# Optimization experiments

Measured on AMD Instinct MI355X. Metric: run time of the kernel, lower is better.

The kernel has to match this reference:

```python
import jax, jax.numpy as jnp
import numpy as np

NUM_FREQ = 64
DIM_OUTPUT = 512
CONST_INV_SOFTMAX = 1e-05


def setup_inputs() -> dict:
    key = jax.random.key(0)
    k1, k2, k3 = jax.random.split(key, 3)
    dim_input = 1024
    L = NUM_FREQ + 1
    batch = jax.random.normal(k1, (16, 4096, dim_input), dtype=jnp.float32)
    # nn.Linear default init (~U[-1/sqrt(fan_in), 1/sqrt(fan_in)]) then divided by 100
    bound = 1.0 / np.sqrt(dim_input)
    W = jax.random.uniform(k2, (2 * L, dim_input), minval=-bound, maxval=bound, dtype=jnp.float32) / 100.0
    b = jax.random.uniform(k3, (2 * L,), minval=-bound, maxval=bound, dtype=jnp.float32) / 100.0
    return {"batch": batch, "W": W, "b": b}


def _autocorrelate(a):
    # a: [B, L] complex. r[k] = sum_j a[j+k] * conj(a[j]), k = 0..L-1.
    # Equivalent to the grouped conv1d in the original; computed via zero-padded FFT.
    L = a.shape[-1]
    X = jnp.fft.fft(a, n=2 * L, axis=-1)
    r = jnp.fft.ifft(X * jnp.conj(X), axis=-1)
    return r[:, :L]


def reference(batch, W, b):
    L = NUM_FREQ + 1
    shape_out = batch.shape[:-1] + (DIM_OUTPUT,)
    x = batch.reshape(-1, batch.shape[-1])              # [B, d_in]
    p = x @ W.T + b                                      # [B, 2L]
    a = jax.lax.complex(p[:, :L], p[:, L:])              # [B, L] complex64
    r = _autocorrelate(a)                                # [B, L] fourier coeffs
    c = r[:, 1:] / r[:, :1].real                         # normalized coeffs [B, F]
    # bin centerpoints on [-1, 1]
    edges = jnp.linspace(-1.0, 1.0, DIM_OUTPUT + 1)
    centers = (edges[:-1] + edges[1:]) / 2               # [D]
    freqs = jnp.pi * jnp.arange(1, L, dtype=jnp.float32) # [F]
    phase = centers[:, None] * freqs[None, :]            # [D, F]
    # Re( sum_f c[b,f] * exp(i*phase[d,f]) ) = c.re @ cos - c.im @ sin
    like = 0.5 + c.real @ jnp.cos(phase).T - c.imag @ jnp.sin(phase).T  # [B, D]
    dist = like / jnp.sum(like, axis=-1, keepdims=True)
    logits = jnp.log(dist + CONST_INV_SOFTMAX)
    return logits.reshape(shape_out)
```

## Files before the change

### kernel.cpp

```cpp
#include <hip/hip_runtime.h>
#include <hip/hip_bf16.h>
#include <math.h>

#define BDIM 1024
#define NP   130
#define LL   65
#define NPAD 144
#define KP2  160
#define DOUT 512

typedef __attribute__((ext_vector_type(4))) float f32x4;
typedef __attribute__((ext_vector_type(8))) __bf16 bf16x8;

__global__ void fill_wbf(const float* __restrict__ W, __bf16* __restrict__ Wbf) {
  int idx = blockIdx.x * 256 + threadIdx.x;
  int c = idx >> 10, k = idx & 1023;
  float v = (c < NP) ? W[c * BDIM + k] : 0.f;
  Wbf[idx] = (__bf16)v;
}

__global__ void fill_mt(__bf16* __restrict__ Mt) {
  int idx = blockIdx.x * 256 + threadIdx.x;
  int col = idx / KP2, k = idx - col * KP2;
  int d = col >> 1, im = col & 1;
  float v = 0.f;
  if (k < NP) {
    int j = (k < LL) ? k : k - LL;
    double theta = M_PI * (-1.0 + (2.0 * (double)d + 1.0) / 512.0);
    double ph = (double)j * theta;
    double s = sin(ph), c = cos(ph);
    v = (float)((k < LL) ? (im ? s : c) : (im ? c : -s));
  }
  Mt[idx] = (__bf16)v;
}

__global__ __launch_bounds__(256) void gemm1(
    const float* __restrict__ X, const __bf16* __restrict__ Wbf,
    const float* __restrict__ bias, __bf16* __restrict__ P,
    float* __restrict__ R0) {
  const int tid  = threadIdx.x;
  const int w    = tid >> 6;
  const int lane = tid & 63;
  const int l15  = lane & 15;
  const int quad = lane >> 4;
  const long rowbase = (long)blockIdx.x * 128 + w * 32;

  f32x4 acc[2][9];
#pragma unroll
  for (int rt = 0; rt < 2; rt++)
#pragma unroll
    for (int j = 0; j < 9; j++) acc[rt][j] = (f32x4){0.f, 0.f, 0.f, 0.f};

  const float*  xptr = X   + (rowbase + l15) * BDIM + quad * 8;
  const __bf16* wptr = Wbf + (long)l15 * BDIM + quad * 8;

  for (int k0 = 0; k0 < BDIM; k0 += 32) {
    bf16x8 a[2];
#pragma unroll
    for (int rt = 0; rt < 2; rt++) {
      f32x4 x0 = *(const f32x4*)(xptr + (long)rt * 16 * BDIM + k0);
      f32x4 x1 = *(const f32x4*)(xptr + (long)rt * 16 * BDIM + k0 + 4);
      bf16x8 af;
      af[0] = (__bf16)x0[0]; af[1] = (__bf16)x0[1];
      af[2] = (__bf16)x0[2]; af[3] = (__bf16)x0[3];
      af[4] = (__bf16)x1[0]; af[5] = (__bf16)x1[1];
      af[6] = (__bf16)x1[2]; af[7] = (__bf16)x1[3];
      a[rt] = af;
    }
#pragma unroll
    for (int j = 0; j < 9; j++) {
      bf16x8 b = *(const bf16x8*)(wptr + (long)j * 16 * BDIM + k0);
      acc[0][j] = __builtin_amdgcn_mfma_f32_16x16x32_bf16(a[0], b, acc[0][j], 0, 0, 0);
      acc[1][j] = __builtin_amdgcn_mfma_f32_16x16x32_bf16(a[1], b, acc[1][j], 0, 0, 0);
    }
  }

  float s[2][4];
#pragma unroll
  for (int rt = 0; rt < 2; rt++)
#pragma unroll
    for (int reg = 0; reg < 4; reg++) s[rt][reg] = 0.f;

#pragma unroll
  for (int j = 0; j < 9; j++) {
    int c = j * 16 + l15;
    float bj = (c < NP) ? bias[c] : 0.f;
#pragma unroll
    for (int rt = 0; rt < 2; rt++) {
#pragma unroll
      for (int reg = 0; reg < 4; reg++) {
        long row = rowbase + rt * 16 + quad * 4 + reg;
        float pv = acc[rt][j][reg] + bj;
        if (c >= NP) pv = 0.f;
        P[row * KP2 + c] = (__bf16)pv;
        s[rt][reg] = fmaf(pv, pv, s[rt][reg]);
      }
    }
  }
#pragma unroll
  for (int rt = 0; rt < 2; rt++)
#pragma unroll
    for (int reg = 0; reg < 4; reg++) {
      long row = rowbase + rt * 16 + quad * 4 + reg;
      P[row * KP2 + NPAD + l15] = (__bf16)0.f;
    }
#pragma unroll
  for (int rt = 0; rt < 2; rt++)
#pragma unroll
    for (int reg = 0; reg < 4; reg++) {
      float v = s[rt][reg];
      v += __shfl_xor(v, 1);
      v += __shfl_xor(v, 2);
      v += __shfl_xor(v, 4);
      v += __shfl_xor(v, 8);
      if (l15 == 0) {
        long row = rowbase + rt * 16 + quad * 4 + reg;
        R0[row] = 1.0f / (512.0f * v);
      }
    }
}

__global__ __launch_bounds__(256) void gemm2(
    const __bf16* __restrict__ P, const __bf16* __restrict__ Mt,
    const float* __restrict__ R0, float* __restrict__ out) {
  const int tid  = threadIdx.x;
  const int w    = tid >> 6;
  const int wr   = w >> 1, wc = w & 1;
  const int lane = tid & 63;
  const int l15  = lane & 15;
  const int quad = lane >> 4;
  const long rowbase = (long)blockIdx.x * 128 + wr * 64;
  const int  colbase = blockIdx.y * 128 + wc * 64;

  f32x4 acc[4][4];
#pragma unroll
  for (int rt = 0; rt < 4; rt++)
#pragma unroll
    for (int ct = 0; ct < 4; ct++) acc[rt][ct] = (f32x4){0.f, 0.f, 0.f, 0.f};

  const __bf16* pptr = P  + (rowbase + l15) * KP2 + quad * 8;
  const __bf16* mptr = Mt + (long)(colbase + l15) * KP2 + quad * 8;

#pragma unroll
  for (int k0 = 0; k0 < KP2; k0 += 32) {
    bf16x8 a[4], b[4];
#pragma unroll
    for (int t = 0; t < 4; t++) a[t] = *(const bf16x8*)(pptr + (long)t * 16 * KP2 + k0);
#pragma unroll
    for (int t = 0; t < 4; t++) b[t] = *(const bf16x8*)(mptr + (long)t * 16 * KP2 + k0);
#pragma unroll
    for (int rt = 0; rt < 4; rt++)
#pragma unroll
      for (int ct = 0; ct < 4; ct++)
        acc[rt][ct] = __builtin_amdgcn_mfma_f32_16x16x32_bf16(a[rt], b[ct], acc[rt][ct], 0, 0, 0);
  }

  const int par = lane & 1;
#pragma unroll
  for (int rt = 0; rt < 4; rt++) {
#pragma unroll
    for (int ct = 0; ct < 4; ct++) {
      const int d = (colbase >> 1) + ct * 8 + (l15 >> 1);
      float t[4];
#pragma unroll
      for (int reg = 0; reg < 4; reg++) {
        float v = acc[rt][ct][reg];
        t[reg] = v * v;
        t[reg] += __shfl_xor(t[reg], 1);
      }
#pragma unroll
      for (int q = 0; q < 2; q++) {
        int reg = par * 2 + q;
        long row = rowbase + rt * 16 + quad * 4 + reg;
        float inv = R0[row];
        out[row * DOUT + d] = __logf(fmaf(t[reg], inv, 1e-5f));
      }
    }
  }
}

extern "C" void kernel_launch(void* const* d_in, const int* in_sizes, int n_in,
                              void* d_out, int out_size, void* d_ws, size_t ws_size,
                              hipStream_t stream) {
  const float* X    = (const float*)d_in[0];
  const float* W    = (const float*)d_in[1];
  const float* bias = (const float*)d_in[2];
  float* out = (float*)d_out;
  const int B = in_sizes[0] / BDIM;

  char* ws = (char*)d_ws;
  __bf16* P   = (__bf16*)ws;                         ws += (size_t)B * KP2 * 2;
  __bf16* Wbf = (__bf16*)ws;                         ws += (size_t)NPAD * BDIM * 2;
  __bf16* Mt  = (__bf16*)ws;                         ws += (size_t)BDIM * KP2 * 2;
  float*  R0  = (float*)ws;

  fill_wbf<<<(NPAD * BDIM) / 256, 256, 0, stream>>>(W, Wbf);
  fill_mt<<<(BDIM * KP2) / 256, 256, 0, stream>>>(Mt);
  gemm1<<<B / 128, 256, 0, stream>>>(X, Wbf, bias, P, R0);
  gemm2<<<dim3(B / 128, 8), 256, 0, stream>>>(P, Mt, R0, out);
}
```

Measured before the change: 522.4 us.

## Halve gemm1 rows per wave, prefetch next X tile, hoist R0 loads, dedupe trig

```diff
diff --git a/kernel.cpp b/kernel.cpp
--- a/kernel.cpp
+++ b/kernel.cpp
@@ -21,17 +21,23 @@
 
 __global__ void fill_mt(__bf16* __restrict__ Mt) {
   int idx = blockIdx.x * 256 + threadIdx.x;
-  int col = idx / KP2, k = idx - col * KP2;
-  int d = col >> 1, im = col & 1;
-  float v = 0.f;
-  if (k < NP) {
-    int j = (k < LL) ? k : k - LL;
+  int d = idx / 80, jj = idx - d * 80;
+  __bf16* col0 = Mt + (size_t)(2 * d) * KP2;
+  __bf16* col1 = Mt + (size_t)(2 * d + 1) * KP2;
+  if (jj < LL) {
     double theta = M_PI * (-1.0 + (2.0 * (double)d + 1.0) / 512.0);
-    double ph = (double)j * theta;
+    double ph = (double)jj * theta;
     double s = sin(ph), c = cos(ph);
-    v = (float)((k < LL) ? (im ? s : c) : (im ? c : -s));
-  }
-  Mt[idx] = (__bf16)v;
+    col0[jj]      = (__bf16)(float)c;
+    col1[jj]      = (__bf16)(float)s;
+    col0[LL + jj] = (__bf16)(float)(-s);
+    col1[LL + jj] = (__bf16)(float)c;
+  } else {
+    int k = NP + (jj - LL);
+    col0[k] = (__bf16)0.f; col1[k] = (__bf16)0.f;
+    k += 15;
+    col0[k] = (__bf16)0.f; col1[k] = (__bf16)0.f;
+  }
 }
 
 __global__ __launch_bounds__(256) void gemm1(
@@ -43,81 +49,70 @@
   const int lane = tid & 63;
   const int l15  = lane & 15;
   const int quad = lane >> 4;
-  const long rowbase = (long)blockIdx.x * 128 + w * 32;
-
-  f32x4 acc[2][9];
-#pragma unroll
-  for (int rt = 0; rt < 2; rt++)
-#pragma unroll
-    for (int j = 0; j < 9; j++) acc[rt][j] = (f32x4){0.f, 0.f, 0.f, 0.f};
+  const long rowbase = (long)blockIdx.x * 64 + w * 16;
+
+  f32x4 acc[9];
+#pragma unroll
+  for (int j = 0; j < 9; j++) acc[j] = (f32x4){0.f, 0.f, 0.f, 0.f};
 
   const float*  xptr = X   + (rowbase + l15) * BDIM + quad * 8;
   const __bf16* wptr = Wbf + (long)l15 * BDIM + quad * 8;
 
+  f32x4 x0 = *(const f32x4*)(xptr);
+  f32x4 x1 = *(const f32x4*)(xptr + 4);
+
+#pragma unroll 2
   for (int k0 = 0; k0 < BDIM; k0 += 32) {
-    bf16x8 a[2];
-#pragma unroll
-    for (int rt = 0; rt < 2; rt++) {
-      f32x4 x0 = *(const f32x4*)(xptr + (long)rt * 16 * BDIM + k0);
-      f32x4 x1 = *(const f32x4*)(xptr + (long)rt * 16 * BDIM + k0 + 4);
-      bf16x8 af;
-      af[0] = (__bf16)x0[0]; af[1] = (__bf16)x0[1];
-      af[2] = (__bf16)x0[2]; af[3] = (__bf16)x0[3];
-      af[4] = (__bf16)x1[0]; af[5] = (__bf16)x1[1];
-      af[6] = (__bf16)x1[2]; af[7] = (__bf16)x1[3];
-      a[rt] = af;
-    }
+    const int kn = (k0 + 32 < BDIM) ? (k0 + 32) : k0;
+    f32x4 n0 = *(const f32x4*)(xptr + kn);
+    f32x4 n1 = *(const f32x4*)(xptr + kn + 4);
+
+    bf16x8 a;
+    a[0] = (__bf16)x0[0]; a[1] = (__bf16)x0[1];
+    a[2] = (__bf16)x0[2]; a[3] = (__bf16)x0[3];
+    a[4] = (__bf16)x1[0]; a[5] = (__bf16)x1[1];
+    a[6] = (__bf16)x1[2]; a[7] = (__bf16)x1[3];
+
 #pragma unroll
     for (int j = 0; j < 9; j++) {
       bf16x8 b = *(const bf16x8*)(wptr + (long)j * 16 * BDIM + k0);
-      acc[0][j] = __builtin_amdgcn_mfma_f32_16x16x32_bf16(a[0], b, acc[0][j], 0, 0, 0);
-      acc[1][j] = __builtin_amdgcn_mfma_f32_16x16x32_bf16(a[1], b, acc[1][j], 0, 0, 0);
-    }
-  }
-
-  float s[2][4];
-#pragma unroll
-  for (int rt = 0; rt < 2; rt++)
-#pragma unroll
-    for (int reg = 0; reg < 4; reg++) s[rt][reg] = 0.f;
+      acc[j] = __builtin_amdgcn_mfma_f32_16x16x32_bf16(a, b, acc[j], 0, 0, 0);
+    }
+    x0 = n0; x1 = n1;
+  }
+
+  float s[4] = {0.f, 0.f, 0.f, 0.f};
 
 #pragma unroll
   for (int j = 0; j < 9; j++) {
     int c = j * 16 + l15;
     float bj = (c < NP) ? bias[c] : 0.f;
 #pragma unroll
-    for (int rt = 0; rt < 2; rt++) {
-#pragma unroll
-      for (int reg = 0; reg < 4; reg++) {
-        long row = rowbase + rt * 16 + quad * 4 + reg;
-        float pv = acc[rt][j][reg] + bj;
-        if (c >= NP) pv = 0.f;
-        P[row * KP2 + c] = (__bf16)pv;
-        s[rt][reg] = fmaf(pv, pv, s[rt][reg]);
-      }
-    }
-  }
-#pragma unroll
-  for (int rt = 0; rt < 2; rt++)
-#pragma unroll
     for (int reg = 0; reg < 4; reg++) {
-      long row = rowbase + rt * 16 + quad * 4 + reg;
-      P[row * KP2 + NPAD + l15] = (__bf16)0.f;
-    }
-#pragma unroll
-  for (int rt = 0; rt < 2; rt++)
-#pragma unroll
-    for (int reg = 0; reg < 4; reg++) {
-      float v = s[rt][reg];
-      v += __shfl_xor(v, 1);
-      v += __shfl_xor(v, 2);
-      v += __shfl_xor(v, 4);
-      v += __shfl_xor(v, 8);
-      if (l15 == 0) {
-        long row = rowbase + rt * 16 + quad * 4 + reg;
-        R0[row] = 1.0f / (512.0f * v);
-      }
-    }
+      long row = rowbase + quad * 4 + reg;
+      float pv = acc[j][reg] + bj;
+      if (c >= NP) pv = 0.f;
+      P[row * KP2 + c] = (__bf16)pv;
+      s[reg] = fmaf(pv, pv, s[reg]);
+    }
+  }
+#pragma unroll
+  for (int reg = 0; reg < 4; reg++) {
+    long row = rowbase + quad * 4 + reg;
+    P[row * KP2 + NPAD + l15] = (__bf16)0.f;
+  }
+#pragma unroll
+  for (int reg = 0; reg < 4; reg++) {
+    float v = s[reg];
+    v += __shfl_xor(v, 1);
+    v += __shfl_xor(v, 2);
+    v += __shfl_xor(v, 4);
+    v += __shfl_xor(v, 8);
+    if (l15 == 0) {
+      long row = rowbase + quad * 4 + reg;
+      R0[row] = 1.0f / (512.0f * v);
+    }
+  }
 }
 
 __global__ __launch_bounds__(256) void gemm2(
@@ -156,6 +151,13 @@
   }
 
   const int par = lane & 1;
+  float inv[4][2];
+#pragma unroll
+  for (int rt = 0; rt < 4; rt++)
+#pragma unroll
+    for (int q = 0; q < 2; q++)
+      inv[rt][q] = R0[rowbase + rt * 16 + quad * 4 + par * 2 + q];
+
 #pragma unroll
   for (int rt = 0; rt < 4; rt++) {
 #pragma unroll
@@ -172,8 +174,7 @@
       for (int q = 0; q < 2; q++) {
         int reg = par * 2 + q;
         long row = rowbase + rt * 16 + quad * 4 + reg;
-        float inv = R0[row];
-        out[row * DOUT + d] = __logf(fmaf(t[reg], inv, 1e-5f));
+        out[row * DOUT + d] = __logf(fmaf(t[reg], inv[rt][q], 1e-5f));
       }
     }
   }
@@ -195,7 +196,7 @@
   float*  R0  = (float*)ws;
 
   fill_wbf<<<(NPAD * BDIM) / 256, 256, 0, stream>>>(W, Wbf);
-  fill_mt<<<(BDIM * KP2) / 256, 256, 0, stream>>>(Mt);
-  gemm1<<<B / 128, 256, 0, stream>>>(X, Wbf, bias, P, R0);
+  fill_mt<<<(512 * 80) / 256, 256, 0, stream>>>(Mt);
+  gemm1<<<B / 64, 256, 0, stream>>>(X, Wbf, bias, P, R0);
   gemm2<<<dim3(B / 128, 8), 256, 0, stream>>>(P, Mt, R0, out);
 }
```

After: 544.1 us. 1.04x slower.
